# Kernel optimization log

Hardware: AMD Instinct MI355X
Metric: run time of the kernel (lower is better)

The kernel has to match this reference:

```python
import jax, jax.numpy as jnp
import numpy as np

IN_CH = 384
HEAD_DIM = 32
MAX_SEQ = 64          # P, tokens per window
N_HEADS = IN_CH // HEAD_DIM
PART = int(np.sqrt(MAX_SEQ))  # 8, window side
SCALE = HEAD_DIM ** -0.5


def _relative_position_index():
    # Swin relative position index, [P*P] int
    h = np.arange(PART)
    coords = np.stack(np.meshgrid(h, h, indexing='ij')).reshape(2, -1)  # [2, P]
    rel = coords[:, :, None] - coords[:, None, :]                        # [2, P, P]
    rel = rel.transpose(1, 2, 0).astype(np.int64)
    rel[:, :, 0] += PART - 1
    rel[:, :, 1] += PART - 1
    rel[:, :, 0] *= 2 * PART - 1
    return rel.sum(-1).reshape(-1)  # [P*P]

REL_IDX = jnp.asarray(_relative_position_index())


def setup_inputs() -> dict:
    key = jax.random.key(0)
    ks = jax.random.split(key, 6)
    B, G, P, D = 32, 64, MAX_SEQ, IN_CH
    x = jax.random.normal(ks[0], (B, G, P, D), dtype=jnp.float32)
    Wqkv = jax.random.normal(ks[1], (D, 3 * D), dtype=jnp.float32) * (D ** -0.5)
    bqkv = jnp.zeros((3 * D,), dtype=jnp.float32)
    Wm = jax.random.normal(ks[2], (D, D), dtype=jnp.float32) * (D ** -0.5)
    bm = jnp.zeros((D,), dtype=jnp.float32)
    # torch init is zeros; use small normal so bias actually affects the output
    rel_table = jax.random.normal(ks[3], ((2 * PART - 1) ** 2, N_HEADS), dtype=jnp.float32) * 0.02
    return {"x": x, "Wqkv": Wqkv, "bqkv": bqkv, "Wm": Wm, "bm": bm, "rel_table": rel_table}


def reference(x, Wqkv, bqkv, Wm, bm, rel_table):
    B, G, P, D = x.shape
    H, DH = N_HEADS, HEAD_DIM
    qkv = x @ Wqkv + bqkv                                   # [B,G,P,3D]
    q, k, v = jnp.split(qkv, 3, axis=-1)
    q = q.reshape(B, G, P, H, DH) * SCALE
    k = k.reshape(B, G, P, H, DH)
    v = v.reshape(B, G, P, H, DH)
    attn = jnp.einsum('bgihd,bgjhd->bghij', q, k)           # [B,G,H,P,P]
    bias = rel_table[REL_IDX].reshape(P, P, H).transpose(2, 0, 1)  # [H,P,P]
    attn = jax.nn.softmax(attn + bias[None, None], axis=-1)
    out = jnp.einsum('bghij,bgjhd->bgihd', attn, v)         # [B,G,P,H,DH]
    out = out.reshape(B, G, P, D)
    return out @ Wm + bm
```

## Files before the change

### kernel.cpp

```cpp
#include <hip/hip_runtime.h>
#include <stdint.h>


typedef __attribute__((ext_vector_type(4))) float f32x4;
typedef __attribute__((ext_vector_type(4))) short s16x4;
typedef __attribute__((ext_vector_type(8))) short s16x8;

#define DEVI static __device__ __forceinline__

DEVI unsigned short f2bf(float f) {
  union { float f; uint32_t u; } v; v.f = f;
  return (unsigned short)((v.u + 0x7FFFu + ((v.u >> 16) & 1u)) >> 16);
}

DEVI uint32_t pk2(float lo, float hi) {
  return (uint32_t)f2bf(lo) | ((uint32_t)f2bf(hi) << 16);
}

DEVI f32x4 zero4() { f32x4 z; z[0] = 0.f; z[1] = 0.f; z[2] = 0.f; z[3] = 0.f; return z; }

#if defined(__has_builtin)
#if __has_builtin(__builtin_amdgcn_mfma_f32_16x16x16bf16_1k)
#define MFMA16_BUILTIN 1
#endif
#if __has_builtin(__builtin_amdgcn_global_load_lds)
#define HAS_GLLDS 1
#endif
#endif

DEVI f32x4 mfma16(s16x4 a, s16x4 b, f32x4 c) {
#ifdef MFMA16_BUILTIN
  return __builtin_amdgcn_mfma_f32_16x16x16bf16_1k(a, b, c, 0, 0, 0);
#else
  asm volatile("v_mfma_f32_16x16x16_bf16 %0, %1, %2, %0" : "+v"(c) : "v"(a), "v"(b));
  return c;
#endif
}

DEVI f32x4 mfma32(s16x8 a, s16x8 b, f32x4 c) {
  return __builtin_amdgcn_mfma_f32_16x16x32_bf16(a, b, c, 0, 0, 0);
}

DEVI void stage1k(const unsigned short* g_lane, unsigned short* lds_base) {
#ifdef HAS_GLLDS
  __builtin_amdgcn_global_load_lds(
      (const __attribute__((address_space(1))) unsigned int*)g_lane,
      (__attribute__((address_space(3))) unsigned int*)lds_base, 16, 0, 0);
#else
  *(s16x8*)(lds_base + (threadIdx.x & 63) * 8) = *(const s16x8*)g_lane;
#endif
}

__global__ void fill_val(float* o, int n, float v) {
  int t = blockIdx.x * 256 + threadIdx.x;
  if (t < n) o[t] = v;
}

__global__ __launch_bounds__(256) void prep_all(
    const float* __restrict__ x, unsigned short* __restrict__ xb,
    const float* __restrict__ Wqkv, unsigned short* __restrict__ WqkvT,
    const float* __restrict__ Wm, unsigned short* __restrict__ WmT,
    const float* __restrict__ bqkv, float* __restrict__ bqkvs,
    const float* __restrict__ rel, float* __restrict__ biasF) {
  const int b = blockIdx.x;
  if (b < 2048) {
    const size_t nchunk = 131072UL * 384 / 8;
    for (size_t i = (size_t)b * 256 + threadIdx.x; i < nchunk; i += 2048UL * 256) {
      f32x4 a = *(const f32x4*)(x + i * 8);
      f32x4 c = *(const f32x4*)(x + i * 8 + 4);
      s16x8 p;
      p[0] = (short)f2bf(a[0]); p[1] = (short)f2bf(a[1]);
      p[2] = (short)f2bf(a[2]); p[3] = (short)f2bf(a[3]);
      p[4] = (short)f2bf(c[0]); p[5] = (short)f2bf(c[1]);
      p[6] = (short)f2bf(c[2]); p[7] = (short)f2bf(c[3]);
      *(s16x8*)(xb + i * 8) = p;
    }
  } else if (b == 2048) {
    for (int t = threadIdx.x; t < 1152; t += 256)
      bqkvs[t] = bqkv[t] * ((t < 384) ? 0.17677669529663687f : 1.0f);
  } else if (b < 2097) {
    int t = (b - 2049) * 256 + threadIdx.x;
    if (t < 12288) {
      int h = t >> 10;
      int r = (t >> 6) & 15;
      int lane = t & 63;
      int jt = r >> 2, it = r & 3;
      int lg = lane >> 4, lr = lane & 15;
      int i = it * 16 + lr;
#pragma unroll
      for (int e = 0; e < 4; ++e) {
        int j = jt * 16 + lg * 4 + e;
        int idx = ((i >> 3) - (j >> 3) + 7) * 15 + ((i & 7) - (j & 7) + 7);
        biasF[t * 4 + e] = rel[idx * 12 + h];
      }
    }
  } else if (b < 2673) {
    int t = (b - 2097) * 256 + threadIdx.x;
    int n = t / 384, k = t - n * 384;
    WmT[t] = f2bf(Wm[(size_t)k * 384 + n]);
  } else {
    int t = (b - 2673) * 256 + threadIdx.x;
    int n = t / 384, k = t - n * 384;
    float s = (n < 384) ? 0.17677669529663687f : 1.0f;
    WqkvT[t] = f2bf(Wqkv[(size_t)k * 1152 + n] * s);
  }
}

template <bool QKV_EPI>
__global__ __launch_bounds__(512, 4) void gemm_k(const unsigned short* __restrict__ A,
                                                 const unsigned short* __restrict__ BT,
                                                 const float* __restrict__ bias,
                                                 void* __restrict__ Cv) {
  constexpr int K = 384;
  constexpr int NT = QKV_EPI ? 9 : 3;
  constexpr int N = NT * 128;
  __shared__ unsigned short sm[2][16384];
  const int bid = blockIdx.x;
  const int swz = (bid & 7) * (NT * 128) + (bid >> 3);
  const int n0 = (swz % NT) * 128;
  const int m0 = (swz / NT) * 128;
  const int tid = threadIdx.x;
  const int lane = tid & 63, wv = tid >> 6;
  const int wr = wv >> 2, wc = wv & 3;
  const int lg = lane >> 4, lr = lane & 15;

  const int scol = ((lane & 7) ^ (lane >> 3)) * 8;
  const unsigned short* Ag = A + (size_t)(m0 + wv * 16 + (lane >> 3)) * K + scol;
  const unsigned short* Bg = BT + (size_t)(n0 + wv * 16 + (lane >> 3)) * K + scol;

  f32x4 acc[4][2];
#pragma unroll
  for (int i = 0; i < 4; ++i)
#pragma unroll
    for (int j = 0; j < 2; ++j) acc[i][j] = zero4();

  auto STAGE = [&](int buf, int k0) {
#pragma unroll
    for (int c2 = 0; c2 < 2; ++c2)
      stage1k(Ag + (size_t)(c2 * 8) * K + k0, &sm[buf][(wv * 16 + c2 * 8) * 64]);
#pragma unroll
    for (int c2 = 0; c2 < 2; ++c2)
      stage1k(Bg + (size_t)(c2 * 8) * K + k0, &sm[buf][8192 + (wv * 16 + c2 * 8) * 64]);
  };
  const int sa = (lr & 7) << 3;
  auto COMPUTE = [&](int buf) {
#pragma unroll
    for (int kk = 0; kk < 64; kk += 32) {
      s16x8 af[4], bf[2];
#pragma unroll
      for (int mt = 0; mt < 4; ++mt)
        af[mt] = *(const s16x8*)&sm[buf][(wr * 64 + 16 * mt + lr) * 64 + ((kk + 8 * lg) ^ sa)];
#pragma unroll
      for (int nt = 0; nt < 2; ++nt)
        bf[nt] = *(const s16x8*)&sm[buf][8192 + (wc * 32 + 16 * nt + lr) * 64 + ((kk + 8 * lg) ^ sa)];
#pragma unroll
      for (int mt = 0; mt < 4; ++mt)
#pragma unroll
        for (int nt = 0; nt < 2; ++nt)
          acc[mt][nt] = mfma32(af[mt], bf[nt], acc[mt][nt]);
    }
  };

  STAGE(0, 0);
  int cur = 0;
#pragma unroll 1
  for (int t = 0; t < 5; ++t) {
    STAGE(cur ^ 1, (t + 1) * 64);
    asm volatile("s_waitcnt vmcnt(4)" ::: "memory");
    __builtin_amdgcn_sched_barrier(0);
    __builtin_amdgcn_s_barrier();
    __builtin_amdgcn_sched_barrier(0);
    COMPUTE(cur);
    __builtin_amdgcn_sched_barrier(0);
    __builtin_amdgcn_s_barrier();
    cur ^= 1;
  }
  asm volatile("s_waitcnt vmcnt(0)" ::: "memory");
  __builtin_amdgcn_sched_barrier(0);
  __builtin_amdgcn_s_barrier();
  __builtin_amdgcn_sched_barrier(0);
  COMPUTE(cur);

  const int crow = m0 + wr * 64 + 4 * lg;
  const int ccol = n0 + wc * 32 + lr;
  if constexpr (QKV_EPI) {
    const int sel = n0 / 384;
    unsigned short* qkv = (unsigned short*)Cv;
    if (sel < 2) {
      unsigned short* tile = &sm[0][0];
#pragma unroll
      for (int nt = 0; nt < 2; ++nt) {
        const int cc = wc * 32 + 16 * nt + lr;
        const float bv = bias[n0 + cc];
#pragma unroll
        for (int mt = 0; mt < 4; ++mt) {
#pragma unroll
          for (int e = 0; e < 4; ++e) {
            const int r = wr * 64 + 16 * mt + 4 * lg + e;
            tile[r * 128 + (cc ^ ((r & 7) << 3))] = f2bf(acc[mt][nt][e] + bv);
          }
        }
      }
      __syncthreads();
      const int hbase = (n0 - sel * 384) >> 5;
      const int tr = wv * 16 + (lane >> 2);
      const int gtok = m0 + tr;
      const int w2 = gtok >> 6, t0r = gtok & 63;
#pragma unroll
      for (int hh = 0; hh < 4; ++hh) {
        const int chunk = hh * 4 + (lane & 3);
        s16x8 v = *(const s16x8*)&tile[tr * 128 + ((chunk * 8) ^ ((tr & 7) << 3))];
        unsigned short* dst = qkv + (((size_t)w2 * 12 + hbase + hh) * 3 + sel) * 2048 +
                              t0r * 32 + (lane & 3) * 8;
        *(s16x8*)dst = v;
      }
    } else {
      const int window = crow >> 6;
      const int t0 = crow & 63;
#pragma unroll
      for (int nt = 0; nt < 2; ++nt) {
        const int col = ccol + 16 * nt;
        const int hcol = col - 768;
        const int h = hcol >> 5, d = hcol & 31;
        const float bv = bias[col];
        unsigned short* base = qkv + (((size_t)window * 12 + h) * 3 + 2) * 2048;
#pragma unroll
        for (int mt = 0; mt < 4; ++mt) {
          s16x4 pk;
#pragma unroll
          for (int e = 0; e < 4; ++e) pk[e] = (short)f2bf(acc[mt][nt][e] + bv);
          *(s16x4*)&base[d * 64 + t0 + 16 * mt] = pk;
        }
      }
    }
  } else {
    float* C = (float*)Cv;
#pragma unroll
    for (int mt = 0; mt < 4; ++mt)
#pragma unroll
      for (int nt = 0; nt < 2; ++nt) {
        const int col = ccol + 16 * nt;
        const float bv = bias[col];
#pragma unroll
        for (int e = 0; e < 4; ++e)
          C[(size_t)(crow + 16 * mt + e) * N + col] = acc[mt][nt][e] + bv;
      }
  }
}

__global__ __launch_bounds__(256) void attn_k(const unsigned short* __restrict__ qkv,
                                              const float* __restrict__ biasF,
                                              unsigned short* __restrict__ attnout) {
  const int lane = threadIdx.x & 63;
  const int wv = threadIdx.x >> 6;
  const int wh = blockIdx.x * 4 + wv;
  const int window = wh / 12;
  const int h = wh - window * 12;
  const int lg = lane >> 4, lr = lane & 15;

  const unsigned short* hb = qkv + (size_t)wh * 6144;
  const unsigned short* Qh = hb;
  const unsigned short* Kh = hb + 2048;
  const unsigned short* Vth = hb + 4096;

  s16x8 ka[4], qb[4];
#pragma unroll
  for (int jt = 0; jt < 4; ++jt)
    ka[jt] = *(const s16x8*)&Kh[(jt * 16 + lr) * 32 + 8 * lg];
#pragma unroll
  for (int it = 0; it < 4; ++it)
    qb[it] = *(const s16x8*)&Qh[(it * 16 + lr) * 32 + 8 * lg];

  f32x4 c[4][4];
#pragma unroll
  for (int a = 0; a < 4; ++a)
#pragma unroll
    for (int b2 = 0; b2 < 4; ++b2) c[a][b2] = zero4();

#pragma unroll
  for (int jt = 0; jt < 4; ++jt)
#pragma unroll
    for (int it = 0; it < 4; ++it)
      c[jt][it] = mfma32(ka[jt], qb[it], c[jt][it]);

  const f32x4* bF = (const f32x4*)biasF + ((size_t)h * 16) * 64 + lane;
#pragma unroll
  for (int jt = 0; jt < 4; ++jt)
#pragma unroll
    for (int it = 0; it < 4; ++it)
      c[jt][it] += bF[(jt * 4 + it) * 64];

  s16x4 pb[4][4];
#pragma unroll
  for (int it = 0; it < 4; ++it) {
    float m = -3.0e38f;
#pragma unroll
    for (int jt = 0; jt < 4; ++jt)
#pragma unroll
      for (int e = 0; e < 4; ++e) m = fmaxf(m, c[jt][it][e]);
    m = fmaxf(m, __shfl_xor(m, 16));
    m = fmaxf(m, __shfl_xor(m, 32));
    float s = 0.f;
#pragma unroll
    for (int jt = 0; jt < 4; ++jt)
#pragma unroll
      for (int e = 0; e < 4; ++e) {
        float p = __expf(c[jt][it][e] - m);
        c[jt][it][e] = p;
        s += p;
      }
    s += __shfl_xor(s, 16);
    s += __shfl_xor(s, 32);
    const float inv = 1.f / s;
#pragma unroll
    for (int jt = 0; jt < 4; ++jt) {
      s16x4 pk;
#pragma unroll
      for (int e = 0; e < 4; ++e) pk[e] = (short)f2bf(c[jt][it][e] * inv);
      pb[jt][it] = pk;
    }
  }

  f32x4 o[2][4];
#pragma unroll
  for (int a = 0; a < 2; ++a)
#pragma unroll
    for (int b2 = 0; b2 < 4; ++b2) o[a][b2] = zero4();

#pragma unroll
  for (int jt = 0; jt < 4; ++jt) {
    s16x4 va[2];
#pragma unroll
    for (int dt = 0; dt < 2; ++dt)
      va[dt] = *(const s16x4*)&Vth[(dt * 16 + lr) * 64 + jt * 16 + 4 * lg];
#pragma unroll
    for (int dt = 0; dt < 2; ++dt)
#pragma unroll
      for (int it = 0; it < 4; ++it)
        o[dt][it] = mfma16(va[dt], pb[jt][it], o[dt][it]);
  }

  unsigned short* ob = attnout + (size_t)window * 64 * 384;
#pragma unroll
  for (int it = 0; it < 4; ++it) {
    const uint32_t p0 = pk2(o[0][it][0], o[0][it][1]);
    const uint32_t p1 = pk2(o[0][it][2], o[0][it][3]);
    const uint32_t q0 = pk2(o[1][it][0], o[1][it][1]);
    const uint32_t q1 = pk2(o[1][it][2], o[1][it][3]);

    const uint32_t x16_0 = __shfl_xor((int)(lg == 2 ? q0 : p0), 16);
    const uint32_t x16_1 = __shfl_xor((int)(lg == 2 ? q1 : p1), 16);
    const uint32_t x32_0 = __shfl_xor((int)(lg == 0 ? q0 : p0), 32);
    const uint32_t x32_1 = __shfl_xor((int)(lg == 0 ? q1 : p1), 32);
    const uint32_t x48_0 = __shfl_xor((int)(lg == 1 ? q0 : p0), 48);
    const uint32_t x48_1 = __shfl_xor((int)(lg == 1 ? q1 : p1), 48);

    uint32_t w[4];
    w[0] = lg == 0 ? p0 : lg == 1 ? x48_0 : lg == 2 ? x32_0 : x16_0;
    w[1] = lg == 0 ? p1 : lg == 1 ? x48_1 : lg == 2 ? x32_1 : x16_1;
    w[2] = lg == 0 ? x16_0 : lg == 1 ? x32_0 : lg == 2 ? x48_0 : q0;
    w[3] = lg == 0 ? x16_1 : lg == 1 ? x32_1 : lg == 2 ? x48_1 : q1;

    *(uint4*)&ob[(size_t)(it * 16 + lr) * 384 + h * 32 + 8 * lg] =
        make_uint4(w[0], w[1], w[2], w[3]);
  }
}

extern "C" void kernel_launch(void* const* d_in, const int* in_sizes, int n_in,
                              void* d_out, int out_size, void* d_ws, size_t ws_size,
                              hipStream_t stream) {
  const float* x = (const float*)d_in[0];
  const float* Wqkv = (const float*)d_in[1];
  const float* bqkv = (const float*)d_in[2];
  const float* Wm = (const float*)d_in[3];
  const float* bm = (const float*)d_in[4];
  const float* rel = (const float*)d_in[5];

  const size_t M = 131072;
  char* ws = (char*)d_ws;
  size_t off = 0;
  unsigned short* qkv = (unsigned short*)(ws + off);   off += M * 1152 * 2;
  unsigned short* xb = (unsigned short*)(ws + off);    off += M * 384 * 2;
  unsigned short* WqkvT = (unsigned short*)(ws + off); off += 1152 * 384 * 2;
  unsigned short* WmT = (unsigned short*)(ws + off);   off += 384 * 384 * 2;
  float* biasF = (float*)(ws + off);                   off += 12 * 16 * 64 * 4 * 4;
  float* bqkvs = (float*)(ws + off);                   off += 1152 * 4;
  unsigned short* attnout = xb;

  if (ws_size < off) {
    fill_val<<<(out_size + 255) / 256, 256, 0, stream>>>((float*)d_out, out_size, 12345.0f);
    return;
  }

  prep_all<<<4401, 256, 0, stream>>>(x, xb, Wqkv, WqkvT, Wm, WmT, bqkv, bqkvs, rel, biasF);
  gemm_k<true><<<9216, 512, 0, stream>>>(xb, WqkvT, bqkvs, qkv);
  attn_k<<<6144, 256, 0, stream>>>(qkv, biasF, attnout);
  gemm_k<false><<<3072, 512, 0, stream>>>(attnout, WmT, bm, d_out);
}
```

Before: 442.5 us.

## Fuse attention with output projection GEMM via shared-memory staging per window

Each block now handles one whole window, with 12 waves (one per head). The attention output goes into padded LDS instead of a global bf16 buffer, and the same block then does the 64x384x384 output projection straight from LDS, adding bias and writing fp32. This removes one kernel launch and the global round trip of the attention output. In exchange, WmT is re-read from L2 by every block, and the projection is done with small per-window tiles rather than the larger tiled GEMM. The larger 768-thread blocks plus about 50KB of LDS may also lower occupancy.

```diff
diff --git a/kernel.cpp b/kernel.cpp
--- a/kernel.cpp
+++ b/kernel.cpp
@@ -248,17 +248,19 @@
   }
 }
 
-__global__ __launch_bounds__(256) void attn_k(const unsigned short* __restrict__ qkv,
-                                              const float* __restrict__ biasF,
-                                              unsigned short* __restrict__ attnout) {
+__global__ __launch_bounds__(768) void attn_gemm2_k(const unsigned short* __restrict__ qkv,
+                                                    const float* __restrict__ biasF,
+                                                    const unsigned short* __restrict__ WmT,
+                                                    const float* __restrict__ bm,
+                                                    float* __restrict__ out) {
+  __shared__ unsigned short att_s[64 * 392];
   const int lane = threadIdx.x & 63;
   const int wv = threadIdx.x >> 6;
-  const int wh = blockIdx.x * 4 + wv;
-  const int window = wh / 12;
-  const int h = wh - window * 12;
+  const int window = blockIdx.x;
+  const int h = wv;
   const int lg = lane >> 4, lr = lane & 15;
 
-  const unsigned short* hb = qkv + (size_t)wh * 6144;
+  const unsigned short* hb = qkv + ((size_t)window * 12 + h) * 6144;
   const unsigned short* Qh = hb;
   const unsigned short* Kh = hb + 2048;
   const unsigned short* Vth = hb + 4096;
@@ -340,7 +342,6 @@
         o[dt][it] = mfma16(va[dt], pb[jt][it], o[dt][it]);
   }
 
-  unsigned short* ob = attnout + (size_t)window * 64 * 384;
 #pragma unroll
   for (int it = 0; it < 4; ++it) {
     const uint32_t p0 = pk2(o[0][it][0], o[0][it][1]);
@@ -361,9 +362,46 @@
     w[2] = lg == 0 ? x16_0 : lg == 1 ? x32_0 : lg == 2 ? x48_0 : q0;
     w[3] = lg == 0 ? x16_1 : lg == 1 ? x32_1 : lg == 2 ? x48_1 : q1;
 
-    *(uint4*)&ob[(size_t)(it * 16 + lr) * 384 + h * 32 + 8 * lg] =
+    *(uint4*)&att_s[(size_t)(it * 16 + lr) * 392 + h * 32 + 8 * lg] =
         make_uint4(w[0], w[1], w[2], w[3]);
   }
+
+  __syncthreads();
+
+  f32x4 acc[4][2];
+#pragma unroll
+  for (int mt = 0; mt < 4; ++mt)
+#pragma unroll
+    for (int nt = 0; nt < 2; ++nt) acc[mt][nt] = zero4();
+
+  const int n0w = wv * 32;
+#pragma unroll 2
+  for (int ks = 0; ks < 12; ++ks) {
+    s16x8 af[4], bf[2];
+#pragma unroll
+    for (int mt = 0; mt < 4; ++mt)
+      af[mt] = *(const s16x8*)&att_s[(16 * mt + lr) * 392 + ks * 32 + 8 * lg];
+#pragma unroll
+    for (int nt = 0; nt < 2; ++nt)
+      bf[nt] = *(const s16x8*)&WmT[(size_t)(n0w + 16 * nt + lr) * 384 + ks * 32 + 8 * lg];
+#pragma unroll
+    for (int mt = 0; mt < 4; ++mt)
+#pragma unroll
+      for (int nt = 0; nt < 2; ++nt)
+        acc[mt][nt] = mfma32(af[mt], bf[nt], acc[mt][nt]);
+  }
+
+  float* ob = out + (size_t)window * 64 * 384;
+#pragma unroll
+  for (int mt = 0; mt < 4; ++mt)
+#pragma unroll
+    for (int nt = 0; nt < 2; ++nt) {
+      const int col = n0w + 16 * nt + lr;
+      const float bv = bm[col];
+#pragma unroll
+      for (int e = 0; e < 4; ++e)
+        ob[(size_t)(16 * mt + 4 * lg + e) * 384 + col] = acc[mt][nt][e] + bv;
+    }
 }
 
 extern "C" void kernel_launch(void* const* d_in, const int* in_sizes, int n_in,
@@ -385,7 +423,6 @@
   unsigned short* WmT = (unsigned short*)(ws + off);   off += 384 * 384 * 2;
   float* biasF = (float*)(ws + off);                   off += 12 * 16 * 64 * 4 * 4;
   float* bqkvs = (float*)(ws + off);                   off += 1152 * 4;
-  unsigned short* attnout = xb;
 
   if (ws_size < off) {
     fill_val<<<(out_size + 255) / 256, 256, 0, stream>>>((float*)d_out, out_size, 12345.0f);
@@ -394,6 +431,5 @@
 
   prep_all<<<4401, 256, 0, stream>>>(x, xb, Wqkv, WqkvT, Wm, WmT, bqkv, bqkvs, rel, biasF);
   gemm_k<true><<<9216, 512, 0, stream>>>(xb, WqkvT, bqkvs, qkv);
-  attn_k<<<6144, 256, 0, stream>>>(qkv, biasF, attnout);
-  gemm_k<false><<<3072, 512, 0, stream>>>(attnout, WmT, bm, d_out);
-}
+  attn_gemm2_k<<<2048, 768, 0, stream>>>(qkv, biasF, WmT, bm, (float*)d_out);
+}
```

After: 424.8 us, median of 3. 1.04x faster.
